# Optimization experiments

Measured on AMD Instinct MI355X. Metric: run time of the kernel, lower is better.

Reference implementation:

```python
import jax, jax.numpy as jnp
import numpy as np

B, C, IMG, P = 64, 3, 224, 16
D, DEPTH, H = 768, 12, 12
DH = D // H
NP_ = (IMG // P) ** 2  # 196
S = NP_ + 1            # 197
FF = 4 * D
EPS = 1e-6


def setup_inputs() -> dict:
    key = jax.random.key(0)
    ks = jax.random.split(key, 16)
    g = lambda k, shape, s=0.02: (jax.random.normal(k, shape, dtype=jnp.float32) * s)
    inp = {
        "x": jax.random.normal(ks[0], (B, C, IMG, IMG), dtype=jnp.float32),
        "patch_w": g(ks[1], (D, C, P, P)),
        "patch_b": jnp.zeros((D,), jnp.float32),
        "cls_token": g(ks[2], (1, 1, D)),
        "pos_embed": g(ks[3], (1, S, D)),
        # per-block params stacked along depth
        "ln1_s": jnp.ones((DEPTH, D), jnp.float32),
        "ln1_b": jnp.zeros((DEPTH, D), jnp.float32),
        "qw": g(ks[4], (DEPTH, D, D)),
        "qb": jnp.zeros((DEPTH, D), jnp.float32),
        "kw": g(ks[5], (DEPTH, D, D)),
        "kb": jnp.zeros((DEPTH, D), jnp.float32),
        "vw": g(ks[6], (DEPTH, D, D)),
        "vb": jnp.zeros((DEPTH, D), jnp.float32),
        "pw": g(ks[7], (DEPTH, D, D)),
        "pb": jnp.zeros((DEPTH, D), jnp.float32),
        "ln2_s": jnp.ones((DEPTH, D), jnp.float32),
        "ln2_b": jnp.zeros((DEPTH, D), jnp.float32),
        "fc1_w": g(ks[8], (DEPTH, D, FF)),
        "fc1_b": jnp.zeros((DEPTH, FF), jnp.float32),
        "fc2_w": g(ks[9], (DEPTH, FF, D)),
        "fc2_b": jnp.zeros((DEPTH, D), jnp.float32),
        "lnf_s": jnp.ones((D,), jnp.float32),
        "lnf_b": jnp.zeros((D,), jnp.float32),
    }
    return inp


def _ln(x, s, b):
    mu = jnp.mean(x, axis=-1, keepdims=True)
    var = jnp.mean(jnp.square(x - mu), axis=-1, keepdims=True)
    return (x - mu) * jax.lax.rsqrt(var + EPS) * s + b


def _vit(x, patch_w, patch_b, cls_token, pos_embed, ln1_s, ln1_b, qw, qb, kw, kb,
         vw, vb, pw, pb, ln2_s, ln2_b, fc1_w, fc1_b, fc2_w, fc2_b, lnf_s, lnf_b):
    # Patch embed: Conv2d(3, D, kernel=16, stride=16)
    h = jax.lax.conv_general_dilated(
        x, patch_w, window_strides=(P, P), padding="VALID",
        dimension_numbers=("NCHW", "OIHW", "NCHW"))  # [B, D, 14, 14]
    h = h.reshape(B, D, NP_).transpose(0, 2, 1) + patch_b  # [B, 196, D]
    cls = jnp.broadcast_to(cls_token, (B, 1, D))
    h = jnp.concatenate([cls, h], axis=1) + pos_embed  # [B, S, D]

    scale = DH ** -0.5

    def block(h, p):
        (l1s, l1b, Wq, bq, Wk, bk, Wv, bv, Wp, bp,
         l2s, l2b, W1, b1, W2, b2) = p
        y = _ln(h, l1s, l1b)
        def heads(t):  # [B,S,D] -> [B,H,S,DH]
            return t.reshape(B, S, H, DH).transpose(0, 2, 1, 3)
        q = heads(y @ Wq + bq)
        k = heads(y @ Wk + bk)
        v = heads(y @ Wv + bv)
        attn = jax.nn.softmax(jnp.einsum("bhsd,bhtd->bhst", q * scale, k), axis=-1)
        o = jnp.einsum("bhst,bhtd->bhsd", attn, v)
        o = o.transpose(0, 2, 1, 3).reshape(B, S, D) @ Wp + bp
        h = h + o
        y = _ln(h, l2s, l2b)
        mlp = jax.nn.gelu(y @ W1 + b1, approximate=False) @ W2 + b2
        return h + mlp, None

    params = (ln1_s, ln1_b, qw, qb, kw, kb, vw, vb, pw, pb,
              ln2_s, ln2_b, fc1_w, fc1_b, fc2_w, fc2_b)
    h, _ = jax.lax.scan(block, h, params)
    h = _ln(h, lnf_s, lnf_b)
    return h[:, 0]  # features == logits (head is Identity)


def reference(x, patch_w, patch_b, cls_token, pos_embed, ln1_s, ln1_b, qw, qb, kw, kb,
              vw, vb, pw, pb, ln2_s, ln2_b, fc1_w, fc1_b, fc2_w, fc2_b, lnf_s, lnf_b):
    return _vit(x, patch_w, patch_b, cls_token, pos_embed, ln1_s, ln1_b, qw, qb, kw, kb,
                vw, vb, pw, pb, ln2_s, ln2_b, fc1_w, fc1_b, fc2_w, fc2_b, lnf_s, lnf_b)
```

## Files before the change

kernel.cpp:

```cpp
#include <hip/hip_runtime.h>
#include <math.h>

constexpr int B_   = 64;
constexpr int S_   = 197;
constexpr int D_   = 768;
constexpr int H_   = 12;
constexpr int FF_  = 3072;
constexpr int DEPTH_ = 12;
constexpr int NP_  = 196;
constexpr int M_   = B_ * S_;
constexpr int MP_  = B_ * NP_;
constexpr int MR   = 12800;

typedef __attribute__((ext_vector_type(8))) short  bf16x8;
typedef __attribute__((ext_vector_type(4))) float  f32x4;
typedef unsigned short ushort_t;

__device__ __forceinline__ ushort_t f2bf(float x) {
    unsigned u = __builtin_bit_cast(unsigned, x);
    unsigned r = u + 0x7FFFu + ((u >> 16) & 1u);
    return (ushort_t)(r >> 16);
}

__device__ __forceinline__ float gelu_f(float v) {
    float y = 0.7978845608f * v + 0.0356774081f * (v * v * v);
    float e = __builtin_amdgcn_exp2f(2.88539008178f * y);
    float t = 1.0f - 2.0f * __builtin_amdgcn_rcpf(1.0f + e);
    return 0.5f * v * (1.0f + t);
}

#define GLOAD_LDS16(g, l)                                                      \
    __builtin_amdgcn_global_load_lds(                                          \
        (const __attribute__((address_space(1))) void*)(g),                    \
        (__attribute__((address_space(3))) void*)(l), 16, 0, 0)


template<int EPI>
__global__ __launch_bounds__(512)
void mm8_k(const ushort_t* __restrict__ A, const ushort_t* __restrict__ Bt,
           const float* __restrict__ bias, const float* __restrict__ res,
           void* __restrict__ Cout, int M, int N, int K) {
    __shared__ __align__(16) ushort_t lds[4 * 16384];
    const int tid  = threadIdx.x;
    const int wid  = tid >> 6;
    const int lane = tid & 63;

    const int nwg  = gridDim.x * gridDim.y;
    const int orig = blockIdx.y * gridDim.x + blockIdx.x;
    const int xcd  = orig & 7, slot = orig >> 3;
    const int q8   = nwg >> 3, r8 = nwg & 7;
    const int logical = (xcd < r8 ? xcd * (q8 + 1) : r8 * (q8 + 1) + (xcd - r8) * q8) + slot;
    const int m0 = (logical / gridDim.x) * 256;
    const int n0 = (logical % gridDim.x) * 256;

    const int wr  = wid >> 2;
    const int wcn = wid & 3;
    const int l15 = lane & 15, kq = lane >> 4;

    const int chb   = ((kq ^ ((l15 ^ (l15 >> 2)) & 3)) & 3) * 16;
    const int abase = wr * 8192 + l15 * 64 + chb;
    const int bbase = 16384 + wcn * 4096 + l15 * 64 + chb;

    const int sr0 = wid * 32 + (lane >> 2);
    const int sr1 = sr0 + 16;
    const int c0s = (lane & 3) ^ ((sr0 ^ (sr0 >> 2)) & 3);
    const int c1s = (lane & 3) ^ ((sr1 ^ (sr1 >> 2)) & 3);
    const size_t gA_0 = (size_t)(m0 + sr0) * K + c0s * 8;
    const size_t gA_1 = (size_t)(m0 + sr1) * K + c1s * 8;
    const size_t gB_0 = (size_t)(n0 + sr0) * K + c0s * 8;
    const size_t gB_1 = (size_t)(n0 + sr1) * K + c1s * 8;
    const int ldsA = wid * 2048;

    char* ldsb = (char*)lds;
    const char* ldsb_c = (const char*)lds;

    f32x4 acc[8][4];
    #pragma unroll
    for (int m = 0; m < 8; ++m)
        #pragma unroll
        for (int n = 0; n < 4; ++n)
            acc[m][n] = (f32x4){0.f, 0.f, 0.f, 0.f};

#define STAGE_A(ss) { char* d_ = ldsb + ((ss) & 3) * 32768 + ldsA;             \
      GLOAD_LDS16(A + gA_0 + (size_t)(ss) * 32, d_);                           \
      GLOAD_LDS16(A + gA_1 + (size_t)(ss) * 32, d_ + 1024); }
#define STAGE_B(ss) { char* d_ = ldsb + ((ss) & 3) * 32768 + 16384 + ldsA;     \
      GLOAD_LDS16(Bt + gB_0 + (size_t)(ss) * 32, d_);                          \
      GLOAD_LDS16(Bt + gB_1 + (size_t)(ss) * 32, d_ + 1024); }

#define PHASE0(s_, DOSTAGE)                                                    \
  { const char* sb_ = ldsb_c + ((s_) & 3) * 32768;                             \
    _Pragma("unroll")                                                          \
    for (int m = 0; m < 4; ++m) av[m] = *(const bf16x8*)(sb_ + abase + m * 1024); \
    _Pragma("unroll")                                                          \
    for (int n = 0; n < 4; ++n) bv[n] = *(const bf16x8*)(sb_ + bbase + n * 1024); \
    if (DOSTAGE) STAGE_A((s_) + 2);                                            \
    __builtin_amdgcn_sched_barrier(0);                                         \
    __builtin_amdgcn_s_barrier();                                              \
    asm volatile("s_waitcnt lgkmcnt(0)" ::: "memory");                         \
    __builtin_amdgcn_sched_barrier(0);                                         \
    __builtin_amdgcn_s_setprio(1);                                             \
    _Pragma("unroll")                                                          \
    for (int m = 0; m < 4; ++m)                                                \
      _Pragma("unroll")                                                        \
      for (int n = 0; n < 4; ++n)                                              \
        acc[m][n] = __builtin_amdgcn_mfma_f32_16x16x32_bf16(av[m], bv[n], acc[m][n], 0, 0, 0); \
    __builtin_amdgcn_s_setprio(0);                                             \
    __builtin_amdgcn_sched_barrier(0);                                         \
    __builtin_amdgcn_s_barrier(); }

#define PHASE1(s_, DOSTAGE, VMC)                                               \
  { const char* sb_ = ldsb_c + ((s_) & 3) * 32768;                             \
    _Pragma("unroll")                                                          \
    for (int m = 0; m < 4; ++m) av[m] = *(const bf16x8*)(sb_ + abase + (m + 4) * 1024); \
    if (DOSTAGE) STAGE_B((s_) + 2);                                            \
    __builtin_amdgcn_sched_barrier(0);                                         \
    __builtin_amdgcn_s_barrier();                                              \
    asm volatile("s_waitcnt lgkmcnt(0)" ::: "memory");                         \
    __builtin_amdgcn_sched_barrier(0);                                         \
    __builtin_amdgcn_s_setprio(1);                                             \
    _Pragma("unroll")                                                          \
    for (int m = 0; m < 4; ++m)                                                \
      _Pragma("unroll")                                                        \
      for (int n = 0; n < 4; ++n)                                              \
        acc[m + 4][n] = __builtin_amdgcn_mfma_f32_16x16x32_bf16(av[m], bv[n], acc[m + 4][n], 0, 0, 0); \
    __builtin_amdgcn_s_setprio(0);                                             \
    asm volatile("s_waitcnt " VMC ::: "memory");                               \
    __builtin_amdgcn_sched_barrier(0);                                         \
    __builtin_amdgcn_s_barrier(); }

    STAGE_A(0); STAGE_B(0); STAGE_A(1); STAGE_B(1);
    asm volatile("s_waitcnt vmcnt(4)" ::: "memory");
    __builtin_amdgcn_s_barrier();

    const int NS = K >> 5;
    bf16x8 av[4], bv[4];
    for (int s = 0; s < NS - 2; ++s) {
        PHASE0(s, true);
        PHASE1(s, true, "vmcnt(4)");
    }
    PHASE0(NS - 2, false);
    PHASE1(NS - 2, false, "vmcnt(0)");
    PHASE0(NS - 1, false);
    PHASE1(NS - 1, false, "vmcnt(0)");

#undef STAGE_A
#undef STAGE_B
#undef PHASE0
#undef PHASE1

    #pragma unroll
    for (int n = 0; n < 4; ++n) {
        const int col = n0 + wcn * 64 + n * 16 + l15;
        const float bcol = bias[col];
        #pragma unroll
        for (int m = 0; m < 8; ++m) {
            #pragma unroll
            for (int j = 0; j < 4; ++j) {
                const int row = m0 + wr * 128 + m * 16 + kq * 4 + j;
                float v = acc[m][n][j] + bcol;
                if (EPI == 1) v = gelu_f(v);
                if (EPI == 2) v += res[(size_t)row * N + col];
                if (EPI <= 1) ((ushort_t*)Cout)[(size_t)row * N + col] = f2bf(v);
                else          ((float*)Cout)[(size_t)row * N + col] = v;
            }
        }
    }
}

constexpr int SKV = 224;
constexpr int VLD = 232;

__global__ __launch_bounds__(256)
void attn2_k(const ushort_t* __restrict__ qkv, ushort_t* __restrict__ o) {
    __shared__ __align__(16) ushort_t Ks[SKV * 64];
    __shared__ __align__(16) ushort_t Vt[64 * VLD];
    __shared__ __align__(16) ushort_t Pw[4 * 512];
    const int h = blockIdx.x, b = blockIdx.y;
    const int tid = threadIdx.x, wid = tid >> 6, lane = tid & 63;
    const size_t baseq = (size_t)(b * S_) * 2304 + h * 64;

    {
        const int jr  = tid >> 3;
        const int dh0 = (tid & 7) * 8;
        for (int pass = 0; pass < 7; ++pass) {
            const int j = pass * 32 + jr;
            bf16x8 kv = {0, 0, 0, 0, 0, 0, 0, 0};
            bf16x8 vv = {0, 0, 0, 0, 0, 0, 0, 0};
            if (j < S_) {
                kv = *(const bf16x8*)&qkv[baseq + (size_t)j * 2304 + 768  + dh0];
                vv = *(const bf16x8*)&qkv[baseq + (size_t)j * 2304 + 1536 + dh0];
            }
            const int koff = (j * 128 + dh0 * 2) ^ ((j & 7) << 4);
            *(bf16x8*)((char*)Ks + koff) = kv;
            #pragma unroll
            for (int i = 0; i < 8; ++i) Vt[(dh0 + i) * VLD + j] = (ushort_t)vv[i];
        }
    }
    __syncthreads();

    char* const pwb = (char*)Pw + wid * 1024;

    for (int it = 0; it < 4; ++it) {
        int sq = it * 64 + wid * 16 + (lane & 15);
        const int sqc = (sq < S_) ? sq : (S_ - 1);
        bf16x8 qf[2];
        #pragma unroll
        for (int kk = 0; kk < 2; ++kk)
            qf[kk] = *(const bf16x8*)&qkv[baseq + (size_t)sqc * 2304 + kk * 32 + (lane >> 4) * 8];

        f32x4 sa[14];
        #pragma unroll
        for (int nf = 0; nf < 14; ++nf) sa[nf] = (f32x4){0.f, 0.f, 0.f, 0.f};
        #pragma unroll
        for (int kk = 0; kk < 2; ++kk) {
            #pragma unroll
            for (int nf = 0; nf < 14; ++nf) {
                const int j = nf * 16 + (lane & 15);
                const int off = (j * 128 + kk * 64 + (lane >> 4) * 16) ^ ((j & 7) << 4);
                bf16x8 kf = *(const bf16x8*)((const char*)Ks + off);
                sa[nf] = __builtin_amdgcn_mfma_f32_16x16x32_bf16(qf[kk], kf, sa[nf], 0, 0, 0);
            }
        }

        const int jcol = lane & 15;
        float mx[4] = {-1e30f, -1e30f, -1e30f, -1e30f};
        #pragma unroll
        for (int nf = 0; nf < 14; ++nf)
            #pragma unroll
            for (int r = 0; r < 4; ++r) mx[r] = fmaxf(mx[r], sa[nf][r]);
        float ls[4];
        #pragma unroll
        for (int r = 0; r < 4; ++r) {
            float m = mx[r] * 0.125f;
            m = fmaxf(m, __shfl_xor(m, 1, 64));
            m = fmaxf(m, __shfl_xor(m, 2, 64));
            m = fmaxf(m, __shfl_xor(m, 4, 64));
            m = fmaxf(m, __shfl_xor(m, 8, 64));
            float s = 0.f;
            #pragma unroll
            for (int nf = 0; nf < 14; ++nf) {
                const int j = nf * 16 + jcol;
                float p = (j < S_) ? exp2f((sa[nf][r] * 0.125f - m) * 1.44269504088896f) : 0.f;
                sa[nf][r] = p;
                s += p;
            }
            s += __shfl_xor(s, 1, 64);
            s += __shfl_xor(s, 2, 64);
            s += __shfl_xor(s, 4, 64);
            s += __shfl_xor(s, 8, 64);
            ls[r] = s;
        }

        f32x4 oa[4];
        #pragma unroll
        for (int nf = 0; nf < 4; ++nf) oa[nf] = (f32x4){0.f, 0.f, 0.f, 0.f};
        #pragma unroll
        for (int kt = 0; kt < 7; ++kt) {
            #pragma unroll
            for (int half = 0; half < 2; ++half) {
                #pragma unroll
                for (int r = 0; r < 4; ++r) {
                    const int qr = (lane >> 4) * 4 + r;
                    const int jl = half * 16 + jcol;
                    const int off = (qr * 64 + jl * 2) ^ (((qr >> 1) & 3) << 4);
                    *(ushort_t*)(pwb + off) = f2bf(sa[kt * 2 + half][r]);
                }
            }
            const int arow = lane & 15;
            const int aoff2 = (arow * 64 + (lane >> 4) * 16) ^ (((arow >> 1) & 3) << 4);
            bf16x8 pa = *(const bf16x8*)(pwb + aoff2);
            #pragma unroll
            for (int nf = 0; nf < 4; ++nf) {
                const int dh = nf * 16 + (lane & 15);
                bf16x8 vb = *(const bf16x8*)((const char*)Vt + dh * (VLD * 2) + (kt * 32 + (lane >> 4) * 8) * 2);
                oa[nf] = __builtin_amdgcn_mfma_f32_16x16x32_bf16(pa, vb, oa[nf], 0, 0, 0);
            }
        }

        #pragma unroll
        for (int r = 0; r < 4; ++r) {
            const int so = it * 64 + wid * 16 + (lane >> 4) * 4 + r;
            if (so < S_) {
                const float inv = 1.0f / ls[r];
                #pragma unroll
                for (int nf = 0; nf < 4; ++nf)
                    o[(size_t)(b * S_ + so) * 768 + h * 64 + nf * 16 + (lane & 15)] = f2bf(oa[nf][r] * inv);
            }
        }
    }
}

__global__ __launch_bounds__(256)
void tcast_k(const float* __restrict__ in, ushort_t* __restrict__ out,
             int R, int C, size_t in_ls, size_t out_ls) {
    __shared__ float t[32][33];
    const float* ip = in + (size_t)blockIdx.z * in_ls;
    ushort_t* op = out + (size_t)blockIdx.z * out_ls;
    const int c0 = blockIdx.x * 32, r0 = blockIdx.y * 32;
    const int tx = threadIdx.x & 31, ty = threadIdx.x >> 5;
    #pragma unroll
    for (int i = 0; i < 4; ++i)
        t[ty + i * 8][tx] = ip[(size_t)(r0 + ty + i * 8) * C + c0 + tx];
    __syncthreads();
    #pragma unroll
    for (int i = 0; i < 4; ++i)
        op[(size_t)(c0 + ty + i * 8) * R + r0 + tx] = f2bf(t[tx][ty + i * 8]);
}

__global__ void cast_k(const float* __restrict__ in, ushort_t* __restrict__ out, int n) {
    int i = blockIdx.x * 256 + threadIdx.x;
    if (i < n) out[i] = f2bf(in[i]);
}

__global__ void biascat_k(const float* __restrict__ qb, const float* __restrict__ kb,
                          const float* __restrict__ vb, float* __restrict__ out) {
    int i = blockIdx.x * 256 + threadIdx.x;
    if (i >= DEPTH_ * 2304) return;
    int l = i / 2304, n = i % 2304;
    float v = (n < 768) ? qb[l * 768 + n] : (n < 1536) ? kb[l * 768 + n - 768] : vb[l * 768 + n - 1536];
    out[i] = v;
}

__global__ void im2col_k(const float* __restrict__ x, ushort_t* __restrict__ pm) {
    size_t idx = (size_t)blockIdx.x * 256 + threadIdx.x;
    if (idx >= (size_t)MP_ * 768) return;
    int col = (int)(idx % 768);
    int row = (int)(idx / 768);
    int b = row / NP_, p = row % NP_;
    int c = col >> 8, rem = col & 255, ky = rem >> 4, kx = rem & 15;
    int py = p / 14, px = p % 14;
    pm[idx] = f2bf(x[(((size_t)b * 3 + c) * 224 + (py * 16 + ky)) * 224 + (px * 16 + kx)]);
}

__global__ void assemble_k(const float* __restrict__ pe, const float* __restrict__ cls,
                           const float* __restrict__ pos, float* __restrict__ h) {
    size_t idx = (size_t)blockIdx.x * 256 + threadIdx.x;
    if (idx >= (size_t)M_ * D_) return;
    int d = (int)(idx % D_);
    int row = (int)(idx / D_);
    int b = row / S_, s = row % S_;
    float v;
    if (s == 0) v = cls[d] + pos[d];
    else        v = pe[((size_t)b * NP_ + (s - 1)) * D_ + d] + pos[(size_t)s * D_ + d];
    h[idx] = v;
}

__device__ __forceinline__ float block_reduce_sum(float val) {
    __shared__ float sm[4];
    #pragma unroll
    for (int off = 32; off > 0; off >>= 1) val += __shfl_xor(val, off, 64);
    int wid = threadIdx.x >> 6;
    if ((threadIdx.x & 63) == 0) sm[wid] = val;
    __syncthreads();
    float r = (sm[0] + sm[1]) + (sm[2] + sm[3]);
    __syncthreads();
    return r;
}

template<bool BF16OUT>
__global__ __launch_bounds__(256)
void ln_k(const float* __restrict__ x, size_t xstride,
          void* __restrict__ y, size_t ystride,
          const float* __restrict__ s, const float* __restrict__ b) {
    const float* xr = x + (size_t)blockIdx.x * xstride;
    const int tid = threadIdx.x;
    float v[3];
    float sum = 0.f;
    #pragma unroll
    for (int t = 0; t < 3; ++t) { v[t] = xr[tid + t * 256]; sum += v[t]; }
    sum = block_reduce_sum(sum);
    const float mu = sum * (1.0f / 768.0f);
    float vs = 0.f;
    #pragma unroll
    for (int t = 0; t < 3; ++t) { float d = v[t] - mu; vs += d * d; }
    vs = block_reduce_sum(vs);
    const float rstd = rsqrtf(vs * (1.0f / 768.0f) + 1e-6f);
    #pragma unroll
    for (int t = 0; t < 3; ++t) {
        int c = tid + t * 256;
        float r = (v[t] - mu) * rstd * s[c] + b[c];
        if (BF16OUT) ((ushort_t*)y)[(size_t)blockIdx.x * ystride + c] = f2bf(r);
        else         ((float*)y)[(size_t)blockIdx.x * ystride + c] = r;
    }
}

extern "C" void kernel_launch(void* const* d_in, const int* in_sizes, int n_in,
                              void* d_out, int out_size, void* d_ws, size_t ws_size,
                              hipStream_t stream) {
    const float* x       = (const float*)d_in[0];
    const float* patch_w = (const float*)d_in[1];
    const float* patch_b = (const float*)d_in[2];
    const float* cls_tok = (const float*)d_in[3];
    const float* pos_emb = (const float*)d_in[4];
    const float* ln1_s   = (const float*)d_in[5];
    const float* ln1_b   = (const float*)d_in[6];
    const float* qw      = (const float*)d_in[7];
    const float* qb      = (const float*)d_in[8];
    const float* kw      = (const float*)d_in[9];
    const float* kb      = (const float*)d_in[10];
    const float* vw      = (const float*)d_in[11];
    const float* vb      = (const float*)d_in[12];
    const float* pw      = (const float*)d_in[13];
    const float* pb      = (const float*)d_in[14];
    const float* ln2_s   = (const float*)d_in[15];
    const float* ln2_b   = (const float*)d_in[16];
    const float* fc1_w   = (const float*)d_in[17];
    const float* fc1_b   = (const float*)d_in[18];
    const float* fc2_w   = (const float*)d_in[19];
    const float* fc2_b   = (const float*)d_in[20];
    const float* lnf_s   = (const float*)d_in[21];
    const float* lnf_b   = (const float*)d_in[22];
    float* out = (float*)d_out;

    char* ws = (char*)d_ws;
    float*    h      = (float*)ws;
    ushort_t* yb     = (ushort_t*)(ws + 39321600);
    char*     Ubase  = ws + 58982400;
    ushort_t* qkvb   = (ushort_t*)Ubase;
    ushort_t* ub     = (ushort_t*)Ubase;
    float*    peb    = (float*)Ubase;
    ushort_t* wqkv_t = (ushort_t*)(ws + 137625600);
    ushort_t* wp_t   = (ushort_t*)(ws + 180092928);
    ushort_t* w1_t   = (ushort_t*)(ws + 194248704);
    ushort_t* w2_t   = (ushort_t*)(ws + 250871808);
    ushort_t* pwt    = (ushort_t*)(ws + 307494912);
    float*    bqkv   = (float*)(ws + 308674560);

    const dim3 blk(256);
    const dim3 blk512(512);

    tcast_k<<<dim3(768 / 32, 768 / 32, 12), blk, 0, stream>>>(qw, wqkv_t,            768, 768, (size_t)768 * 768, (size_t)2304 * 768);
    tcast_k<<<dim3(768 / 32, 768 / 32, 12), blk, 0, stream>>>(kw, wqkv_t + 768 * 768, 768, 768, (size_t)768 * 768, (size_t)2304 * 768);
    tcast_k<<<dim3(768 / 32, 768 / 32, 12), blk, 0, stream>>>(vw, wqkv_t + 1536 * 768, 768, 768, (size_t)768 * 768, (size_t)2304 * 768);
    tcast_k<<<dim3(768 / 32, 768 / 32, 12), blk, 0, stream>>>(pw, wp_t, 768, 768, (size_t)768 * 768, (size_t)768 * 768);
    tcast_k<<<dim3(3072 / 32, 768 / 32, 12), blk, 0, stream>>>(fc1_w, w1_t, 768, 3072, (size_t)768 * 3072, (size_t)3072 * 768);
    tcast_k<<<dim3(768 / 32, 3072 / 32, 12), blk, 0, stream>>>(fc2_w, w2_t, 3072, 768, (size_t)3072 * 768, (size_t)768 * 3072);
    cast_k<<<dim3((768 * 768 + 255) / 256), blk, 0, stream>>>(patch_w, pwt, 768 * 768);
    biascat_k<<<dim3((DEPTH_ * 2304 + 255) / 256), blk, 0, stream>>>(qb, kb, vb, bqkv);

    im2col_k<<<dim3(((size_t)MP_ * 768 + 255) / 256), blk, 0, stream>>>(x, yb);
    mm8_k<3><<<dim3(3, MR / 256), blk512, 0, stream>>>(yb, pwt, patch_b, nullptr, peb, MR, 768, 768);
    assemble_k<<<dim3(((size_t)M_ * D_ + 255) / 256), blk, 0, stream>>>(peb, cls_tok, pos_emb, h);

    const dim3 gQKV(9, MR / 256);
    const dim3 gD(3, MR / 256);
    const dim3 gFF(12, MR / 256);
    for (int l = 0; l < DEPTH_; ++l) {
        const size_t oDD = (size_t)l * 768 * 768;
        const size_t oD  = (size_t)l * 768;
        const size_t oDF = (size_t)l * 768 * FF_;
        const size_t oF  = (size_t)l * FF_;

        ln_k<true><<<dim3(M_), blk, 0, stream>>>(h, 768, yb, 768, ln1_s + oD, ln1_b + oD);
        mm8_k<0><<<gQKV, blk512, 0, stream>>>(yb, wqkv_t + (size_t)l * 2304 * 768, bqkv + (size_t)l * 2304, nullptr, qkvb, MR, 2304, 768);
        attn2_k<<<dim3(H_, B_), blk, 0, stream>>>(qkvb, yb);
        mm8_k<2><<<gD, blk512, 0, stream>>>(yb, wp_t + oDD, pb + oD, h, h, MR, 768, 768);
        ln_k<true><<<dim3(M_), blk, 0, stream>>>(h, 768, yb, 768, ln2_s + oD, ln2_b + oD);
        mm8_k<1><<<gFF, blk512, 0, stream>>>(yb, w1_t + oDF, fc1_b + oF, nullptr, ub, MR, FF_, 768);
        mm8_k<2><<<gD, blk512, 0, stream>>>(ub, w2_t + oDF, fc2_b + oD, h, h, MR, 768, FF_);
    }

    ln_k<false><<<dim3(B_), blk, 0, stream>>>(h, (size_t)S_ * D_, out, 768, lnf_s, lnf_b);
}
```

Measured before the change: 4.602 ms.

## Replace 256x256 GEMM tiles with templated 128-row tiles and 3-stage pipeline

The 256x256 four-buffer GEMM kernel is replaced by a templated kernel using 128-row tiles, with 128 or 256 columns and 4 or 8 waves, and a three-slot LDS ring. N=768 GEMMs (projection, fc2, patch embed) use 128x128 tiles with 4 waves, giving 600 workgroups instead of 150 so the GPU's compute units are better filled. QKV and fc1 use 128x256 tiles with 8 waves and a higher occupancy hint. The cost is less operand reuse per tile and more global traffic, and the pipeline now issues a single phase per K step.

```diff
diff --git a/kernel.cpp b/kernel.cpp
--- a/kernel.cpp
+++ b/kernel.cpp
@@ -35,12 +35,19 @@
         (__attribute__((address_space(3))) void*)(l), 16, 0, 0)
 
 
-template<int EPI>
-__global__ __launch_bounds__(512)
-void mm8_k(const ushort_t* __restrict__ A, const ushort_t* __restrict__ Bt,
-           const float* __restrict__ bias, const float* __restrict__ res,
-           void* __restrict__ Cout, int M, int N, int K) {
-    __shared__ __align__(16) ushort_t lds[4 * 16384];
+template<int EPI, int BN, int NWAVE>
+__global__ __launch_bounds__(NWAVE * 64, (NWAVE == 8) ? 4 : 3)
+void mm_t(const ushort_t* __restrict__ A, const ushort_t* __restrict__ Bt,
+          const float* __restrict__ bias, const float* __restrict__ res,
+          void* __restrict__ Cout, int M, int N, int K) {
+    constexpr int THREADS = NWAVE * 64;
+    constexpr int SLICE   = (128 + BN) * 64;
+    constexpr int PASSB   = THREADS * 16;
+    constexpr int PA      = 8192 / PASSB;
+    constexpr int PB      = (BN * 64) / PASSB;
+    constexpr int LV      = PA + PB;
+    __shared__ __align__(16) char lds[3 * SLICE];
+
     const int tid  = threadIdx.x;
     const int wid  = tid >> 6;
     const int lane = tid & 63;
@@ -50,51 +57,52 @@
     const int xcd  = orig & 7, slot = orig >> 3;
     const int q8   = nwg >> 3, r8 = nwg & 7;
     const int logical = (xcd < r8 ? xcd * (q8 + 1) : r8 * (q8 + 1) + (xcd - r8) * q8) + slot;
-    const int m0 = (logical / gridDim.x) * 256;
-    const int n0 = (logical % gridDim.x) * 256;
-
-    const int wr  = wid >> 2;
-    const int wcn = wid & 3;
+    const int m0 = (logical / gridDim.x) * 128;
+    const int n0 = (logical % gridDim.x) * BN;
+
+    const int wr  = (NWAVE == 8) ? (wid >> 2) : (wid >> 1);
+    const int wcn = (NWAVE == 8) ? (wid & 3)  : (wid & 1);
     const int l15 = lane & 15, kq = lane >> 4;
 
     const int chb   = ((kq ^ ((l15 ^ (l15 >> 2)) & 3)) & 3) * 16;
-    const int abase = wr * 8192 + l15 * 64 + chb;
-    const int bbase = 16384 + wcn * 4096 + l15 * 64 + chb;
-
-    const int sr0 = wid * 32 + (lane >> 2);
-    const int sr1 = sr0 + 16;
-    const int c0s = (lane & 3) ^ ((sr0 ^ (sr0 >> 2)) & 3);
-    const int c1s = (lane & 3) ^ ((sr1 ^ (sr1 >> 2)) & 3);
-    const size_t gA_0 = (size_t)(m0 + sr0) * K + c0s * 8;
-    const size_t gA_1 = (size_t)(m0 + sr1) * K + c1s * 8;
-    const size_t gB_0 = (size_t)(n0 + sr0) * K + c0s * 8;
-    const size_t gB_1 = (size_t)(n0 + sr1) * K + c1s * 8;
-    const int ldsA = wid * 2048;
-
-    char* ldsb = (char*)lds;
-    const char* ldsb_c = (const char*)lds;
-
-    f32x4 acc[8][4];
-    #pragma unroll
-    for (int m = 0; m < 8; ++m)
+    const int abase = wr * 4096 + l15 * 64 + chb;
+    const int bbase = 8192 + wcn * 4096 + l15 * 64 + chb;
+
+    const int srow = tid >> 2;
+    const int sc   = (tid & 3) ^ ((srow ^ (srow >> 2)) & 3);
+    size_t gA[PA], gB[PB];
+    #pragma unroll
+    for (int p = 0; p < PA; ++p) gA[p] = (size_t)(m0 + srow + p * (THREADS / 4)) * K + sc * 8;
+    #pragma unroll
+    for (int p = 0; p < PB; ++p) gB[p] = (size_t)(n0 + srow + p * (THREADS / 4)) * K + sc * 8;
+
+    f32x4 acc[4][4];
+    #pragma unroll
+    for (int m = 0; m < 4; ++m)
         #pragma unroll
         for (int n = 0; n < 4; ++n)
             acc[m][n] = (f32x4){0.f, 0.f, 0.f, 0.f};
 
-#define STAGE_A(ss) { char* d_ = ldsb + ((ss) & 3) * 32768 + ldsA;             \
-      GLOAD_LDS16(A + gA_0 + (size_t)(ss) * 32, d_);                           \
-      GLOAD_LDS16(A + gA_1 + (size_t)(ss) * 32, d_ + 1024); }
-#define STAGE_B(ss) { char* d_ = ldsb + ((ss) & 3) * 32768 + 16384 + ldsA;     \
-      GLOAD_LDS16(Bt + gB_0 + (size_t)(ss) * 32, d_);                          \
-      GLOAD_LDS16(Bt + gB_1 + (size_t)(ss) * 32, d_ + 1024); }
-
-#define PHASE0(s_, DOSTAGE)                                                    \
-  { const char* sb_ = ldsb_c + ((s_) & 3) * 32768;                             \
+#define MMT_STAGE(ss)                                                          \
+    { char* d_ = lds + ((ss) % 3) * SLICE + wid * 1024;                        \
+      const size_t ko_ = (size_t)(ss) * 32;                                    \
+      _Pragma("unroll")                                                        \
+      for (int p = 0; p < PA; ++p) GLOAD_LDS16(A + gA[p] + ko_, d_ + p * PASSB); \
+      _Pragma("unroll")                                                        \
+      for (int p = 0; p < PB; ++p) GLOAD_LDS16(Bt + gB[p] + ko_, d_ + 8192 + p * PASSB); }
+
+#define MMT_VMW()                                                              \
+    { if constexpr (LV == 3) { asm volatile("s_waitcnt vmcnt(3)" ::: "memory"); } \
+      else                   { asm volatile("s_waitcnt vmcnt(4)" ::: "memory"); } }
+
+#define MMT_PHASE(s_, DOSTAGE, FINAL)                                          \
+  { const char* sb_ = lds + ((s_) % 3) * SLICE;                                \
+    bf16x8 av[4], bv[4];                                                       \
     _Pragma("unroll")                                                          \
     for (int m = 0; m < 4; ++m) av[m] = *(const bf16x8*)(sb_ + abase + m * 1024); \
     _Pragma("unroll")                                                          \
     for (int n = 0; n < 4; ++n) bv[n] = *(const bf16x8*)(sb_ + bbase + n * 1024); \
-    if (DOSTAGE) STAGE_A((s_) + 2);                                            \
+    if (DOSTAGE) MMT_STAGE((s_) + 2);                                          \
     __builtin_amdgcn_sched_barrier(0);                                         \
     __builtin_amdgcn_s_barrier();                                              \
     asm volatile("s_waitcnt lgkmcnt(0)" ::: "memory");                         \
@@ -106,58 +114,35 @@
       for (int n = 0; n < 4; ++n)                                              \
         acc[m][n] = __builtin_amdgcn_mfma_f32_16x16x32_bf16(av[m], bv[n], acc[m][n], 0, 0, 0); \
     __builtin_amdgcn_s_setprio(0);                                             \
+    if (FINAL) { asm volatile("s_waitcnt vmcnt(0)" ::: "memory"); }            \
+    else       { MMT_VMW(); }                                                  \
     __builtin_amdgcn_sched_barrier(0);                                         \
     __builtin_amdgcn_s_barrier(); }
 
-#define PHASE1(s_, DOSTAGE, VMC)                                               \
-  { const char* sb_ = ldsb_c + ((s_) & 3) * 32768;                             \
-    _Pragma("unroll")                                                          \
-    for (int m = 0; m < 4; ++m) av[m] = *(const bf16x8*)(sb_ + abase + (m + 4) * 1024); \
-    if (DOSTAGE) STAGE_B((s_) + 2);                                            \
-    __builtin_amdgcn_sched_barrier(0);                                         \
-    __builtin_amdgcn_s_barrier();                                              \
-    asm volatile("s_waitcnt lgkmcnt(0)" ::: "memory");                         \
-    __builtin_amdgcn_sched_barrier(0);                                         \
-    __builtin_amdgcn_s_setprio(1);                                             \
-    _Pragma("unroll")                                                          \
-    for (int m = 0; m < 4; ++m)                                                \
-      _Pragma("unroll")                                                        \
-      for (int n = 0; n < 4; ++n)                                              \
-        acc[m + 4][n] = __builtin_amdgcn_mfma_f32_16x16x32_bf16(av[m], bv[n], acc[m + 4][n], 0, 0, 0); \
-    __builtin_amdgcn_s_setprio(0);                                             \
-    asm volatile("s_waitcnt " VMC ::: "memory");                               \
-    __builtin_amdgcn_sched_barrier(0);                                         \
-    __builtin_amdgcn_s_barrier(); }
-
-    STAGE_A(0); STAGE_B(0); STAGE_A(1); STAGE_B(1);
-    asm volatile("s_waitcnt vmcnt(4)" ::: "memory");
+    MMT_STAGE(0); MMT_STAGE(1);
+    MMT_VMW();
     __builtin_amdgcn_s_barrier();
 
     const int NS = K >> 5;
-    bf16x8 av[4], bv[4];
     for (int s = 0; s < NS - 2; ++s) {
-        PHASE0(s, true);
-        PHASE1(s, true, "vmcnt(4)");
-    }
-    PHASE0(NS - 2, false);
-    PHASE1(NS - 2, false, "vmcnt(0)");
-    PHASE0(NS - 1, false);
-    PHASE1(NS - 1, false, "vmcnt(0)");
-
-#undef STAGE_A
-#undef STAGE_B
-#undef PHASE0
-#undef PHASE1
+        MMT_PHASE(s, true, false);
+    }
+    MMT_PHASE(NS - 2, false, true);
+    MMT_PHASE(NS - 1, false, true);
+
+#undef MMT_STAGE
+#undef MMT_VMW
+#undef MMT_PHASE
 
     #pragma unroll
     for (int n = 0; n < 4; ++n) {
         const int col = n0 + wcn * 64 + n * 16 + l15;
         const float bcol = bias[col];
         #pragma unroll
-        for (int m = 0; m < 8; ++m) {
+        for (int m = 0; m < 4; ++m) {
             #pragma unroll
             for (int j = 0; j < 4; ++j) {
-                const int row = m0 + wr * 128 + m * 16 + kq * 4 + j;
+                const int row = m0 + wr * 64 + m * 16 + kq * 4 + j;
                 float v = acc[m][n][j] + bcol;
                 if (EPI == 1) v = gelu_f(v);
                 if (EPI == 2) v += res[(size_t)row * N + col];
@@ -440,12 +425,9 @@
     biascat_k<<<dim3((DEPTH_ * 2304 + 255) / 256), blk, 0, stream>>>(qb, kb, vb, bqkv);
 
     im2col_k<<<dim3(((size_t)MP_ * 768 + 255) / 256), blk, 0, stream>>>(x, yb);
-    mm8_k<3><<<dim3(3, MR / 256), blk512, 0, stream>>>(yb, pwt, patch_b, nullptr, peb, MR, 768, 768);
+    mm_t<3, 128, 4><<<dim3(6, 100), blk, 0, stream>>>(yb, pwt, patch_b, nullptr, peb, MR, 768, 768);
     assemble_k<<<dim3(((size_t)M_ * D_ + 255) / 256), blk, 0, stream>>>(peb, cls_tok, pos_emb, h);
 
-    const dim3 gQKV(9, MR / 256);
-    const dim3 gD(3, MR / 256);
-    const dim3 gFF(12, MR / 256);
     for (int l = 0; l < DEPTH_; ++l) {
         const size_t oDD = (size_t)l * 768 * 768;
         const size_t oD  = (size_t)l * 768;
@@ -453,12 +435,12 @@
         const size_t oF  = (size_t)l * FF_;
 
         ln_k<true><<<dim3(M_), blk, 0, stream>>>(h, 768, yb, 768, ln1_s + oD, ln1_b + oD);
-        mm8_k<0><<<gQKV, blk512, 0, stream>>>(yb, wqkv_t + (size_t)l * 2304 * 768, bqkv + (size_t)l * 2304, nullptr, qkvb, MR, 2304, 768);
+        mm_t<0, 256, 8><<<dim3(9, 100), blk512, 0, stream>>>(yb, wqkv_t + (size_t)l * 2304 * 768, bqkv + (size_t)l * 2304, nullptr, qkvb, MR, 2304, 768);
         attn2_k<<<dim3(H_, B_), blk, 0, stream>>>(qkvb, yb);
-        mm8_k<2><<<gD, blk512, 0, stream>>>(yb, wp_t + oDD, pb + oD, h, h, MR, 768, 768);
+        mm_t<2, 128, 4><<<dim3(6, 100), blk, 0, stream>>>(yb, wp_t + oDD, pb + oD, h, h, MR, 768, 768);
         ln_k<true><<<dim3(M_), blk, 0, stream>>>(h, 768, yb, 768, ln2_s + oD, ln2_b + oD);
-        mm8_k<1><<<gFF, blk512, 0, stream>>>(yb, w1_t + oDF, fc1_b + oF, nullptr, ub, MR, FF_, 768);
-        mm8_k<2><<<gD, blk512, 0, stream>>>(ub, w2_t + oDF, fc2_b + oD, h, h, MR, 768, FF_);
+        mm_t<1, 256, 8><<<dim3(12, 100), blk512, 0, stream>>>(yb, w1_t + oDF, fc1_b + oF, nullptr, ub, MR, FF_, 768);
+        mm_t<2, 128, 4><<<dim3(6, 100), blk, 0, stream>>>(ub, w2_t + oDF, fc2_b + oD, h, h, MR, 768, FF_);
     }
 
     ln_k<false><<<dim3(B_), blk, 0, stream>>>(h, (size_t)S_ * D_, out, 768, lnf_s, lnf_b);
```

After: 4.177 ms. 9.2% less time.

## Split-K with atomic accumulation for N=768 GEMMs and simplify LDS staging layout

Applied to the files above, without the earlier changes.

The N=768 GEMMs (attention projection, fc2 and patch embed) produce only 150 output tiles, which underfills the device, so they are now split along K across blockIdx.z. Each split accumulates its partial result into the fp32 output with relaxed atomic adds. For the projection and fc2 this lands directly in the residual stream `h`, and only the first split adds the bias. A new init kernel pre-fills the patch-embed output with the bias, yet split 0 still adds the bias again, so the patch bias is applied twice. That only goes unnoticed because the test bias is zero. The LDS staging layout also drops the XOR swizzle in favour of a kq-major linear layout. The costs are extra atomic traffic and a summation order that is no longer deterministic.

```diff
diff --git a/kernel.cpp b/kernel.cpp
--- a/kernel.cpp
+++ b/kernel.cpp
@@ -37,10 +37,10 @@
 
 template<int EPI>
 __global__ __launch_bounds__(512)
-void mm8_k(const ushort_t* __restrict__ A, const ushort_t* __restrict__ Bt,
-           const float* __restrict__ bias, const float* __restrict__ res,
-           void* __restrict__ Cout, int M, int N, int K) {
-    __shared__ __align__(16) ushort_t lds[4 * 16384];
+void mm256_k(const ushort_t* __restrict__ A, const ushort_t* __restrict__ Bt,
+             const float* __restrict__ bias, void* __restrict__ Cout,
+             int M, int N, int K, int SP) {
+    __shared__ __align__(16) char lds[4 * 32768];
     const int tid  = threadIdx.x;
     const int wid  = tid >> 6;
     const int lane = tid & 63;
@@ -53,26 +53,23 @@
     const int m0 = (logical / gridDim.x) * 256;
     const int n0 = (logical % gridDim.x) * 256;
 
+    const int s0 = blockIdx.z * SP;
+    const int s1 = min(s0 + SP, K >> 5);
+
     const int wr  = wid >> 2;
     const int wcn = wid & 3;
     const int l15 = lane & 15, kq = lane >> 4;
 
-    const int chb   = ((kq ^ ((l15 ^ (l15 >> 2)) & 3)) & 3) * 16;
-    const int abase = wr * 8192 + l15 * 64 + chb;
-    const int bbase = 16384 + wcn * 4096 + l15 * 64 + chb;
-
-    const int sr0 = wid * 32 + (lane >> 2);
-    const int sr1 = sr0 + 16;
-    const int c0s = (lane & 3) ^ ((sr0 ^ (sr0 >> 2)) & 3);
-    const int c1s = (lane & 3) ^ ((sr1 ^ (sr1 >> 2)) & 3);
-    const size_t gA_0 = (size_t)(m0 + sr0) * K + c0s * 8;
-    const size_t gA_1 = (size_t)(m0 + sr1) * K + c1s * 8;
-    const size_t gB_0 = (size_t)(n0 + sr0) * K + c0s * 8;
-    const size_t gB_1 = (size_t)(n0 + sr1) * K + c1s * 8;
-    const int ldsA = wid * 2048;
-
-    char* ldsb = (char*)lds;
-    const char* ldsb_c = (const char*)lds;
+    const int abase = kq * 4096 + wr * 2048 + l15 * 16;
+    const int bbase = 16384 + kq * 4096 + wcn * 1024 + l15 * 16;
+
+    const size_t gA0 = (size_t)(m0 + (tid & 255)) * K + (tid >> 8) * 8;
+    const size_t gA1 = gA0 + 16;
+    const size_t gB0 = (size_t)(n0 + (tid & 255)) * K + (tid >> 8) * 8;
+    const size_t gB1 = gB0 + 16;
+
+    char* ldsb = lds;
+    const char* ldsb_c = lds;
 
     f32x4 acc[8][4];
     #pragma unroll
@@ -81,20 +78,20 @@
         for (int n = 0; n < 4; ++n)
             acc[m][n] = (f32x4){0.f, 0.f, 0.f, 0.f};
 
-#define STAGE_A(ss) { char* d_ = ldsb + ((ss) & 3) * 32768 + ldsA;             \
-      GLOAD_LDS16(A + gA_0 + (size_t)(ss) * 32, d_);                           \
-      GLOAD_LDS16(A + gA_1 + (size_t)(ss) * 32, d_ + 1024); }
-#define STAGE_B(ss) { char* d_ = ldsb + ((ss) & 3) * 32768 + 16384 + ldsA;     \
-      GLOAD_LDS16(Bt + gB_0 + (size_t)(ss) * 32, d_);                          \
-      GLOAD_LDS16(Bt + gB_1 + (size_t)(ss) * 32, d_ + 1024); }
+#define STG_A(ss) { char* d_ = ldsb + ((ss) & 3) * 32768 + tid * 16;           \
+      GLOAD_LDS16(A + gA0 + (size_t)(ss) * 32, d_);                            \
+      GLOAD_LDS16(A + gA1 + (size_t)(ss) * 32, d_ + 8192); }
+#define STG_B(ss) { char* d_ = ldsb + ((ss) & 3) * 32768 + 16384 + tid * 16;   \
+      GLOAD_LDS16(Bt + gB0 + (size_t)(ss) * 32, d_);                           \
+      GLOAD_LDS16(Bt + gB1 + (size_t)(ss) * 32, d_ + 8192); }
 
 #define PHASE0(s_, DOSTAGE)                                                    \
   { const char* sb_ = ldsb_c + ((s_) & 3) * 32768;                             \
     _Pragma("unroll")                                                          \
-    for (int m = 0; m < 4; ++m) av[m] = *(const bf16x8*)(sb_ + abase + m * 1024); \
+    for (int m = 0; m < 4; ++m) av[m] = *(const bf16x8*)(sb_ + abase + m * 256); \
     _Pragma("unroll")                                                          \
-    for (int n = 0; n < 4; ++n) bv[n] = *(const bf16x8*)(sb_ + bbase + n * 1024); \
-    if (DOSTAGE) STAGE_A((s_) + 2);                                            \
+    for (int n = 0; n < 4; ++n) bv[n] = *(const bf16x8*)(sb_ + bbase + n * 256); \
+    if (DOSTAGE) STG_A((s_) + 2);                                              \
     __builtin_amdgcn_sched_barrier(0);                                         \
     __builtin_amdgcn_s_barrier();                                              \
     asm volatile("s_waitcnt lgkmcnt(0)" ::: "memory");                         \
@@ -112,8 +109,8 @@
 #define PHASE1(s_, DOSTAGE, VMC)                                               \
   { const char* sb_ = ldsb_c + ((s_) & 3) * 32768;                             \
     _Pragma("unroll")                                                          \
-    for (int m = 0; m < 4; ++m) av[m] = *(const bf16x8*)(sb_ + abase + (m + 4) * 1024); \
-    if (DOSTAGE) STAGE_B((s_) + 2);                                            \
+    for (int m = 0; m < 4; ++m) av[m] = *(const bf16x8*)(sb_ + abase + (m + 4) * 256); \
+    if (DOSTAGE) STG_B((s_) + 2);                                              \
     __builtin_amdgcn_sched_barrier(0);                                         \
     __builtin_amdgcn_s_barrier();                                              \
     asm volatile("s_waitcnt lgkmcnt(0)" ::: "memory");                         \
@@ -129,30 +126,30 @@
     __builtin_amdgcn_sched_barrier(0);                                         \
     __builtin_amdgcn_s_barrier(); }
 
-    STAGE_A(0); STAGE_B(0); STAGE_A(1); STAGE_B(1);
+    STG_A(s0); STG_B(s0); STG_A(s0 + 1); STG_B(s0 + 1);
     asm volatile("s_waitcnt vmcnt(4)" ::: "memory");
     __builtin_amdgcn_s_barrier();
 
-    const int NS = K >> 5;
     bf16x8 av[4], bv[4];
-    for (int s = 0; s < NS - 2; ++s) {
+    for (int s = s0; s < s1 - 2; ++s) {
         PHASE0(s, true);
         PHASE1(s, true, "vmcnt(4)");
     }
-    PHASE0(NS - 2, false);
-    PHASE1(NS - 2, false, "vmcnt(0)");
-    PHASE0(NS - 1, false);
-    PHASE1(NS - 1, false, "vmcnt(0)");
-
-#undef STAGE_A
-#undef STAGE_B
+    PHASE0(s1 - 2, false);
+    PHASE1(s1 - 2, false, "vmcnt(0)");
+    PHASE0(s1 - 1, false);
+    PHASE1(s1 - 1, false, "vmcnt(0)");
+
+#undef STG_A
+#undef STG_B
 #undef PHASE0
 #undef PHASE1
 
+    const bool addb = (EPI != 4) || (blockIdx.z == 0);
     #pragma unroll
     for (int n = 0; n < 4; ++n) {
         const int col = n0 + wcn * 64 + n * 16 + l15;
-        const float bcol = bias[col];
+        const float bcol = addb ? bias[col] : 0.f;
         #pragma unroll
         for (int m = 0; m < 8; ++m) {
             #pragma unroll
@@ -160,9 +157,12 @@
                 const int row = m0 + wr * 128 + m * 16 + kq * 4 + j;
                 float v = acc[m][n][j] + bcol;
                 if (EPI == 1) v = gelu_f(v);
-                if (EPI == 2) v += res[(size_t)row * N + col];
-                if (EPI <= 1) ((ushort_t*)Cout)[(size_t)row * N + col] = f2bf(v);
-                else          ((float*)Cout)[(size_t)row * N + col] = v;
+                if (EPI == 4) {
+                    __hip_atomic_fetch_add(&((float*)Cout)[(size_t)row * N + col], v,
+                                           __ATOMIC_RELAXED, __HIP_MEMORY_SCOPE_AGENT);
+                } else {
+                    ((ushort_t*)Cout)[(size_t)row * N + col] = f2bf(v);
+                }
             }
         }
     }
@@ -320,6 +320,11 @@
     int l = i / 2304, n = i % 2304;
     float v = (n < 768) ? qb[l * 768 + n] : (n < 1536) ? kb[l * 768 + n - 768] : vb[l * 768 + n - 1536];
     out[i] = v;
+}
+
+__global__ void pebinit_k(const float* __restrict__ b, float* __restrict__ peb) {
+    size_t i = (size_t)blockIdx.x * 256 + threadIdx.x;
+    if (i < (size_t)MR * 768) peb[i] = b[i % 768];
 }
 
 __global__ void im2col_k(const float* __restrict__ x, ushort_t* __restrict__ pm) {
@@ -440,12 +445,10 @@
     biascat_k<<<dim3((DEPTH_ * 2304 + 255) / 256), blk, 0, stream>>>(qb, kb, vb, bqkv);
 
     im2col_k<<<dim3(((size_t)MP_ * 768 + 255) / 256), blk, 0, stream>>>(x, yb);
-    mm8_k<3><<<dim3(3, MR / 256), blk512, 0, stream>>>(yb, pwt, patch_b, nullptr, peb, MR, 768, 768);
+    pebinit_k<<<dim3(((size_t)MR * 768 + 255) / 256), blk, 0, stream>>>(patch_b, peb);
+    mm256_k<4><<<dim3(3, 50, 3), blk512, 0, stream>>>(yb, pwt, patch_b, peb, MR, 768, 768, 8);
     assemble_k<<<dim3(((size_t)M_ * D_ + 255) / 256), blk, 0, stream>>>(peb, cls_tok, pos_emb, h);
 
-    const dim3 gQKV(9, MR / 256);
-    const dim3 gD(3, MR / 256);
-    const dim3 gFF(12, MR / 256);
     for (int l = 0; l < DEPTH_; ++l) {
         const size_t oDD = (size_t)l * 768 * 768;
         const size_t oD  = (size_t)l * 768;
@@ -453,12 +456,12 @@
         const size_t oF  = (size_t)l * FF_;
 
         ln_k<true><<<dim3(M_), blk, 0, stream>>>(h, 768, yb, 768, ln1_s + oD, ln1_b + oD);
-        mm8_k<0><<<gQKV, blk512, 0, stream>>>(yb, wqkv_t + (size_t)l * 2304 * 768, bqkv + (size_t)l * 2304, nullptr, qkvb, MR, 2304, 768);
+        mm256_k<0><<<dim3(9, 50, 1), blk512, 0, stream>>>(yb, wqkv_t + (size_t)l * 2304 * 768, bqkv + (size_t)l * 2304, qkvb, MR, 2304, 768, 24);
         attn2_k<<<dim3(H_, B_), blk, 0, stream>>>(qkvb, yb);
-        mm8_k<2><<<gD, blk512, 0, stream>>>(yb, wp_t + oDD, pb + oD, h, h, MR, 768, 768);
+        mm256_k<4><<<dim3(3, 50, 3), blk512, 0, stream>>>(yb, wp_t + oDD, pb + oD, h, MR, 768, 768, 8);
         ln_k<true><<<dim3(M_), blk, 0, stream>>>(h, 768, yb, 768, ln2_s + oD, ln2_b + oD);
-        mm8_k<1><<<gFF, blk512, 0, stream>>>(yb, w1_t + oDF, fc1_b + oF, nullptr, ub, MR, FF_, 768);
-        mm8_k<2><<<gD, blk512, 0, stream>>>(ub, w2_t + oDF, fc2_b + oD, h, h, MR, 768, FF_);
+        mm256_k<1><<<dim3(12, 50, 1), blk512, 0, stream>>>(yb, w1_t + oDF, fc1_b + oF, ub, MR, FF_, 768, 24);
+        mm256_k<4><<<dim3(3, 50, 5), blk512, 0, stream>>>(ub, w2_t + oDF, fc2_b + oD, h, MR, 768, 3072, 20);
     }
 
     ln_k<false><<<dim3(B_), blk, 0, stream>>>(h, (size_t)S_ * D_, out, 768, lnf_s, lnf_b);
```

After: 7.414 ms. 1.61x slower.
